# Optimization experiments

Measured on AMD Instinct MI355X. Metric: run time of the kernel, lower is better.

The kernel has to match this reference:

```python
import jax, jax.numpy as jnp
import numpy as np

EPS = 1e-5
NUM_GROUPS = 32
NUM_HEADS = 8

def group_norm(x, w, b):
    # x: (B, C, H, W), 32 groups, affine per-channel
    B, C, H, W = x.shape
    xg = x.reshape(B, NUM_GROUPS, C // NUM_GROUPS, H, W)
    mu = xg.mean(axis=(2, 3, 4), keepdims=True)
    var = xg.var(axis=(2, 3, 4), keepdims=True)
    xn = ((xg - mu) * jax.lax.rsqrt(var + EPS)).reshape(B, C, H, W)
    return xn * w[None, :, None, None] + b[None, :, None, None]

def conv1x1(x, w, b):
    # 1x1 conv == per-pixel linear; w: (out, in), x: (B, C, H, W)
    return jnp.einsum('oc,bchw->bohw', w, x) + b[None, :, None, None]

def setup_inputs() -> dict:
    key = jax.random.key(0)
    ks = jax.random.split(key, 4)
    B, C, H, W = 2, 512, 64, 64
    s = 1.0 / np.sqrt(C)
    return {
        'x': jax.random.normal(ks[0], (B, C, H, W), jnp.float32),
        'gn_w': jnp.ones((C,), jnp.float32),
        'gn_b': jnp.zeros((C,), jnp.float32),
        'wq': jax.random.normal(ks[1], (C, C), jnp.float32) * s,
        'bq': jnp.zeros((C,), jnp.float32),
        'wkv': jax.random.normal(ks[2], (2 * C, C), jnp.float32) * s,
        'bkv': jnp.zeros((2 * C,), jnp.float32),
        'wo': jax.random.normal(ks[3], (C, C), jnp.float32) * s,
        'bo': jnp.zeros((C,), jnp.float32),
    }

def reference(x, gn_w, gn_b, wq, bq, wkv, bkv, wo, bo):
    B, C, H, W = x.shape
    hd = C // NUM_HEADS  # head_dim
    residual = x
    x_norm = group_norm(x, gn_w, gn_b)
    q = conv1x1(x_norm, wq, bq).reshape(B, NUM_HEADS, hd, H * W)
    kv = conv1x1(x_norm, wkv, bkv)
    k, v = jnp.split(kv, 2, axis=1)
    k = k.reshape(B, NUM_HEADS, hd, H * W)
    v = v.reshape(B, NUM_HEADS, hd, H * W)
    scale = hd ** (-0.5)
    attn = jnp.einsum('bhdi,bhdj->bhij', q, k) * scale
    attn = jax.nn.softmax(attn, axis=-1)
    out = jnp.einsum('bhij,bhdj->bhdi', attn, v).reshape(B, C, H, W)
    out = conv1x1(out, wo, bo)
    return out + residual
```

## Files before the change

### kernel.cpp

```cpp
#include <hip/hip_runtime.h>
#include <cmath>

typedef __bf16 bf16x8 __attribute__((ext_vector_type(8)));
typedef __bf16 bf16x4 __attribute__((ext_vector_type(4)));
typedef float  f32x4  __attribute__((ext_vector_type(4)));
typedef unsigned uint2_ev __attribute__((ext_vector_type(2)));

static __device__ __forceinline__ f32x4 mfma16(bf16x8 a, bf16x8 b, f32x4 c) {
    return __builtin_amdgcn_mfma_f32_16x16x32_bf16(a, b, c, 0, 0, 0);
}

static __device__ __forceinline__ float fast_exp2(float x) {
#if __has_builtin(__builtin_amdgcn_exp2f)
    return __builtin_amdgcn_exp2f(x);
#else
    return exp2f(x);
#endif
}

static __device__ __forceinline__ void quad_swap(unsigned &a, unsigned &b) {
#if __has_builtin(__builtin_amdgcn_permlane32_swap) && __has_builtin(__builtin_amdgcn_permlane16_swap)
    uint2_ev r32 = __builtin_amdgcn_permlane32_swap(a, b, false, false);
    uint2_ev r16 = __builtin_amdgcn_permlane16_swap(r32[0], r32[1], false, false);
    a = r16[0]; b = r16[1];
#else
    asm volatile("v_permlane32_swap_b32 %0, %1\n\t"
                 "v_permlane16_swap_b32 %0, %1"
                 : "+v"(a), "+v"(b));
#endif
}

static __device__ __forceinline__ void gload_lds16(const void* g, void* l) {
    __builtin_amdgcn_global_load_lds((const __attribute__((address_space(1))) void*)g,
                                     (__attribute__((address_space(3))) void*)l, 16, 0, 0);
}

#define OFF_STATS 0
#define OFF_W     4096
#define OFF_XNT   (OFF_W + 2u*1024*1024)
#define OFF_QKT   (OFF_XNT + 8u*1024*1024)
#define OFF_V     (OFF_QKT + 16u*1024*1024)
#define OFF_OP    (OFF_V + 8u*1024*1024)
#define CHUNK_O   4194304u
#define CHUNK_L   65536u

__global__ __launch_bounds__(256) void cvt_w(const float* __restrict__ wq,
                                             const float* __restrict__ wkv,
                                             const float* __restrict__ wo,
                                             __bf16* __restrict__ dst) {
    int i = blockIdx.x * 256 + threadIdx.x;
    if (i < 262144)      dst[i] = (__bf16)wq[i];
    else if (i < 786432) dst[i] = (__bf16)wkv[i - 262144];
    else                 dst[i] = (__bf16)wo[i - 786432];
}

__global__ __launch_bounds__(256) void gn_stats(const float* __restrict__ x,
                                                float* __restrict__ stats) {
    int blk = blockIdx.x;
    int bg = blk >> 2, chunk = blk & 3;
    const float* base = x + (size_t)bg * 65536 + (size_t)chunk * 16384;
    float s = 0.f, ss = 0.f;
    for (int i = threadIdx.x; i < 4096; i += 256) {
        float4 v = ((const float4*)base)[i];
        s  += v.x + v.y + v.z + v.w;
        ss += v.x*v.x + v.y*v.y + v.z*v.z + v.w*v.w;
    }
    #pragma unroll
    for (int off = 1; off < 64; off <<= 1) {
        s  += __shfl_xor(s,  off);
        ss += __shfl_xor(ss, off);
    }
    __shared__ float red[8];
    int wave = threadIdx.x >> 6;
    if ((threadIdx.x & 63) == 0) { red[wave*2] = s; red[wave*2+1] = ss; }
    __syncthreads();
    if (threadIdx.x == 0) {
        float S  = red[0] + red[2] + red[4] + red[6];
        float SS = red[1] + red[3] + red[5] + red[7];
        atomicAdd(&stats[bg*2],     S);
        atomicAdd(&stats[bg*2 + 1], SS);
    }
}

__global__ __launch_bounds__(256) void gn_apply(const float* __restrict__ x,
                                                const float* __restrict__ stats,
                                                const float* __restrict__ w,
                                                const float* __restrict__ bgn,
                                                __bf16* __restrict__ xnT) {
    int p0 = blockIdx.x * 64, c0 = blockIdx.y * 64, b = blockIdx.z;
    int tid = threadIdx.x, lane = tid & 63, wave = tid >> 6;
    __shared__ float t[64][69];
    #pragma unroll
    for (int i = 0; i < 16; ++i) {
        int cc = i * 4 + wave;
        int c  = c0 + cc;
        int g  = (b << 5) + (c >> 4);
        float mu  = stats[g*2] * (1.f/65536.f);
        float var = stats[g*2+1] * (1.f/65536.f) - mu*mu;
        float rstd = rsqrtf(var + 1e-5f);
        float val = x[((size_t)(b*512 + c) << 12) + p0 + lane];
        t[cc][lane] = (val - mu) * rstd * w[c] + bgn[c];
    }
    __syncthreads();
    #pragma unroll
    for (int i = 0; i < 16; ++i) {
        int pp = i * 4 + wave;
        xnT[((size_t)(b*4096 + p0 + pp) << 9) + c0 + lane] = (__bf16)t[lane][pp];
    }
}

__global__ __launch_bounds__(256) void gemm128_kernel(
    const __bf16* __restrict__ A, const __bf16* __restrict__ B,
    const float* __restrict__ bias, const float* __restrict__ bias2, int nsplit,
    float scale0, void* __restrict__ out,
    int N, int K, long long strideA, long long strideO) {
    const int bz = blockIdx.z;
    A += strideA * bz;
    const int m0 = blockIdx.x * 128, n0 = blockIdx.y * 128;
    const int tid = threadIdx.x, lane = tid & 63, wave = tid >> 6;
    const int quad = lane >> 4, l16 = lane & 15;
    const int wm = (wave >> 1) * 64, wn = (wave & 1) * 64;

    __shared__ __attribute__((aligned(16))) __bf16 lds_a[128][40];
    __shared__ __attribute__((aligned(16))) __bf16 lds_b[128][40];

    f32x4 acc[4][4];
    #pragma unroll
    for (int mt = 0; mt < 4; ++mt)
        #pragma unroll
        for (int nt = 0; nt < 4; ++nt)
            #pragma unroll
            for (int r = 0; r < 4; ++r) acc[mt][nt][r] = 0.f;

    const int row_s = tid >> 2;
    const int kc    = (tid & 3) << 3;

    uint4 ra0, ra1, rb0, rb1;
    const __bf16* Abase = A + (size_t)(m0 + row_s) * K + kc;
    const __bf16* Bbase = B + (size_t)(n0 + row_s) * K + kc;
    ra0 = *(const uint4*)Abase;
    ra1 = *(const uint4*)(Abase + (size_t)64 * K);
    rb0 = *(const uint4*)Bbase;
    rb1 = *(const uint4*)(Bbase + (size_t)64 * K);

    for (int kt = 0; kt < K; kt += 32) {
        *(uint4*)&lds_a[row_s][kc]      = ra0;
        *(uint4*)&lds_a[row_s + 64][kc] = ra1;
        *(uint4*)&lds_b[row_s][kc]      = rb0;
        *(uint4*)&lds_b[row_s + 64][kc] = rb1;
        __syncthreads();
        if (kt + 32 < K) {
            ra0 = *(const uint4*)(Abase + kt + 32);
            ra1 = *(const uint4*)(Abase + kt + 32 + (size_t)64 * K);
            rb0 = *(const uint4*)(Bbase + kt + 32);
            rb1 = *(const uint4*)(Bbase + kt + 32 + (size_t)64 * K);
        }
        bf16x8 af[4], bfr[4];
        #pragma unroll
        for (int mt = 0; mt < 4; ++mt)
            af[mt] = *(const bf16x8*)&lds_a[wm + mt*16 + l16][quad*8];
        #pragma unroll
        for (int nt = 0; nt < 4; ++nt)
            bfr[nt] = *(const bf16x8*)&lds_b[wn + nt*16 + l16][quad*8];
        #pragma unroll
        for (int mt = 0; mt < 4; ++mt)
            #pragma unroll
            for (int nt = 0; nt < 4; ++nt)
                acc[mt][nt] = mfma16(af[mt], bfr[nt], acc[mt][nt]);
        __syncthreads();
    }

    #pragma unroll
    for (int mt = 0; mt < 4; ++mt) {
        const int mrow = m0 + wm + mt*16 + quad*4;
        #pragma unroll
        for (int nt = 0; nt < 4; ++nt) {
            const int ncol = n0 + wn + nt*16 + l16;
            #pragma unroll
            for (int r = 0; r < 4; ++r) {
                const int m = mrow + r;
                float bval = (ncol < nsplit) ? bias[ncol] : bias2[ncol - nsplit];
                float val = acc[mt][nt][r] + bval;
                if (ncol < nsplit) val *= scale0;
                ((__bf16*)out)[(size_t)strideO * bz + (size_t)m * N + ncol] = (__bf16)val;
            }
        }
    }
}

template<int OUT_F32, int HAS_RES>
__global__ __launch_bounds__(256) void gemm64_kernel(
    const __bf16* __restrict__ A, const __bf16* __restrict__ B,
    const float* __restrict__ bias, const float* __restrict__ res,
    void* __restrict__ out,
    int N, int K, long long strideB, long long strideO) {
    const int bz = blockIdx.z;
    B += strideB * bz;
    const int m0 = blockIdx.x * 64, n0 = blockIdx.y * 128;
    const int tid = threadIdx.x, lane = tid & 63, wave = tid >> 6;
    const int quad = lane >> 4, l16 = lane & 15;
    const int wn = wave * 32;

    __shared__ __attribute__((aligned(16))) __bf16 lds_a[64][40];
    __shared__ __attribute__((aligned(16))) __bf16 lds_b[128][40];

    f32x4 acc[4][2];
    #pragma unroll
    for (int mt = 0; mt < 4; ++mt)
        #pragma unroll
        for (int nt = 0; nt < 2; ++nt)
            #pragma unroll
            for (int r = 0; r < 4; ++r) acc[mt][nt][r] = 0.f;

    const int row_s = tid >> 2;
    const int kc    = (tid & 3) << 3;

    uint4 ra0, rb0, rb1;
    const __bf16* Abase = A + (size_t)(m0 + row_s) * K + kc;
    const __bf16* Bbase = B + (size_t)(n0 + row_s) * K + kc;
    ra0 = *(const uint4*)Abase;
    rb0 = *(const uint4*)Bbase;
    rb1 = *(const uint4*)(Bbase + (size_t)64 * K);

    for (int kt = 0; kt < K; kt += 32) {
        *(uint4*)&lds_a[row_s][kc]      = ra0;
        *(uint4*)&lds_b[row_s][kc]      = rb0;
        *(uint4*)&lds_b[row_s + 64][kc] = rb1;
        __syncthreads();
        if (kt + 32 < K) {
            ra0 = *(const uint4*)(Abase + kt + 32);
            rb0 = *(const uint4*)(Bbase + kt + 32);
            rb1 = *(const uint4*)(Bbase + kt + 32 + (size_t)64 * K);
        }
        bf16x8 af[4], bfr[2];
        #pragma unroll
        for (int mt = 0; mt < 4; ++mt)
            af[mt] = *(const bf16x8*)&lds_a[mt*16 + l16][quad*8];
        #pragma unroll
        for (int nt = 0; nt < 2; ++nt)
            bfr[nt] = *(const bf16x8*)&lds_b[wn + nt*16 + l16][quad*8];
        #pragma unroll
        for (int mt = 0; mt < 4; ++mt)
            #pragma unroll
            for (int nt = 0; nt < 2; ++nt)
                acc[mt][nt] = mfma16(af[mt], bfr[nt], acc[mt][nt]);
        __syncthreads();
    }

    #pragma unroll
    for (int mt = 0; mt < 4; ++mt) {
        const int mrow = m0 + mt*16 + quad*4;
        #pragma unroll
        for (int nt = 0; nt < 2; ++nt) {
            const int ncol = n0 + wn + nt*16 + l16;
            #pragma unroll
            for (int r = 0; r < 4; ++r) {
                const int m = mrow + r;
                float val = acc[mt][nt][r] + bias[m];
                const size_t idx = (size_t)strideO * bz + (size_t)m * N + ncol;
                if constexpr (HAS_RES) val += res[idx];
                if constexpr (OUT_F32) ((float*)out)[idx] = val;
                else ((__bf16*)out)[idx] = (__bf16)val;
            }
        }
    }
}

template<int NCH>
__global__ __launch_bounds__(256, 3) void attn_kernel(const __bf16* __restrict__ qkT,
                                                      const __bf16* __restrict__ v,
                                                      __bf16* __restrict__ attnT,
                                                      __bf16* __restrict__ Opart,
                                                      float* __restrict__ Lpart) {
    const int b = blockIdx.y >> 3, h = blockIdx.y & 7;
    const int chunk = (NCH > 1) ? blockIdx.z : 0;
    const int NITER = 64 / NCH;
    const int kt0 = chunk * (4096 / NCH);
    const int tid = threadIdx.x;
    const int wave = tid >> 6, lane = tid & 63;
    const int quad = lane >> 4, l16 = lane & 15;
    const int qbase = blockIdx.x * 256 + wave * 64;

    const __bf16* qkTb = qkT + ((size_t)b << 22);
    const __bf16* vb   = v   + ((size_t)b << 21);

    __shared__ __attribute__((aligned(16))) __bf16 lds_k[2][64][64];
    __shared__ __attribute__((aligned(16))) __bf16 lds_v[2][64][64];

    bf16x8 aq[4][2];
    #pragma unroll
    for (int mt = 0; mt < 4; ++mt) {
        const __bf16* qrow = qkTb + (size_t)(qbase + mt*16 + l16) * 1024 + h*64 + quad*8;
        aq[mt][0] = *(const bf16x8*)qrow;
        aq[mt][1] = *(const bf16x8*)(qrow + 32);
    }
    f32x4 o[4][5];
    #pragma unroll
    for (int mt = 0; mt < 4; ++mt)
        #pragma unroll
        for (int dt = 0; dt < 5; ++dt)
            #pragma unroll
            for (int r = 0; r < 4; ++r) o[mt][dt][r] = 0.f;
    const f32x4 kZero = {0.f, 0.f, 0.f, 0.f};

    bf16x8 onesb;
    #pragma unroll
    for (int e = 0; e < 8; ++e) onesb[e] = (__bf16)1.0f;

    const int myrow = (wave << 3) + (lane >> 3);
    const int mych  = ((lane & 7) ^ (myrow & 7)) << 3;
    const __bf16* kgb = qkTb + (size_t)myrow * 1024 + 512 + h*64 + mych;
    const __bf16* vgb = vb + ((size_t)(h*64 + myrow) << 12) + mych;

    auto stage = [&](int buf, int kt) {
        char* kb = (char*)(&lds_k[buf][0][0]) + (wave << 10);
        char* vp = (char*)(&lds_v[buf][0][0]) + (wave << 10);
        const __bf16* kg = kgb + (size_t)kt * 1024;
        const __bf16* vg = vgb + kt;
        gload_lds16(kg,                       kb);
        gload_lds16(kg + 32*1024,             kb + 4096);
        gload_lds16(vg,                       vp);
        gload_lds16(vg + ((size_t)32 << 12),  vp + 4096);
    };

    stage(0, kt0);

    for (int it = 0; it < NITER; ++it) {
        __syncthreads();
        const int cur = it & 1;
        if (it + 1 < NITER) stage(cur ^ 1, kt0 + (it + 1) * 64);

        #pragma unroll
        for (int kh = 0; kh < 2; ++kh) {
            unsigned pd[4][4];
            #pragma unroll
            for (int j = 0; j < 2; ++j) {
                const int nt = kh*2 + j;
                const int kr = nt*16 + l16;
                bf16x8 bk0 = *(const bf16x8*)&lds_k[cur][kr][( quad      ^ (l16 & 7)) * 8];
                bf16x8 bk1 = *(const bf16x8*)&lds_k[cur][kr][((4 + quad) ^ (l16 & 7)) * 8];
                #pragma unroll
                for (int mt = 0; mt < 4; ++mt) {
                    f32x4 s = mfma16(bk1, aq[mt][1], mfma16(bk0, aq[mt][0], kZero));
                    f32x4 p;
                    #pragma unroll
                    for (int r = 0; r < 4; ++r) p[r] = fast_exp2(s[r]);
                    bf16x4 pb = __builtin_convertvector(p, bf16x4);
                    union { bf16x4 v; unsigned d[2]; } u; u.v = pb;
                    pd[mt][j*2]     = u.d[0];
                    pd[mt][j*2 + 1] = u.d[1];
                }
            }
            bf16x8 pa[4];
            #pragma unroll
            for (int mt = 0; mt < 4; ++mt) {
                unsigned x0 = pd[mt][0], x1 = pd[mt][1];
                unsigned y0 = pd[mt][2], y1 = pd[mt][3];
                quad_swap(x0, y0);
                quad_swap(x1, y1);
                union { unsigned d[4]; bf16x8 v; } u;
                u.d[0] = x0; u.d[1] = x1; u.d[2] = y0; u.d[3] = y1;
                pa[mt] = u.v;
            }
            #pragma unroll
            for (int dt = 0; dt < 4; ++dt) {
                bf16x8 bv = *(const bf16x8*)&lds_v[cur][dt*16 + l16][((kh*4 + quad) ^ (l16 & 7)) * 8];
                #pragma unroll
                for (int mt = 0; mt < 4; ++mt)
                    o[mt][dt] = mfma16(pa[mt], bv, o[mt][dt]);
            }
            #pragma unroll
            for (int mt = 0; mt < 4; ++mt)
                o[mt][4] = mfma16(pa[mt], onesb, o[mt][4]);
        }
    }

    if constexpr (NCH > 1) {
        __bf16* Ob = Opart + (size_t)chunk * CHUNK_O;
        #pragma unroll
        for (int mt = 0; mt < 4; ++mt)
            #pragma unroll
            for (int dt = 0; dt < 4; ++dt)
                #pragma unroll
                for (int r = 0; r < 4; ++r) {
                    size_t row = (size_t)b * 4096 + qbase + mt*16 + quad*4 + r;
                    Ob[(row << 9) + (h << 6) + dt*16 + l16] = (__bf16)o[mt][dt][r];
                }
        if (l16 == 0) {
            #pragma unroll
            for (int mt = 0; mt < 4; ++mt)
                #pragma unroll
                for (int r = 0; r < 4; ++r) {
                    int p = qbase + mt*16 + quad*4 + r;
                    Lpart[(size_t)chunk * CHUNK_L + (size_t)(((b*8 + h)) << 12) + p] = o[mt][4][r];
                }
        }
    } else {
        #pragma unroll
        for (int mt = 0; mt < 4; ++mt) {
            float inv[4];
            #pragma unroll
            for (int r = 0; r < 4; ++r)
                inv[r] = 1.f / __shfl(o[mt][4][r], lane & 48);
            #pragma unroll
            for (int dt = 0; dt < 4; ++dt)
                #pragma unroll
                for (int r = 0; r < 4; ++r) {
                    size_t row = (size_t)b * 4096 + qbase + mt*16 + quad*4 + r;
                    attnT[(row << 9) + (h << 6) + dt*16 + l16] = (__bf16)(o[mt][dt][r] * inv[r]);
                }
        }
    }
}

template<int NCH>
__global__ __launch_bounds__(256) void attn_combine(const __bf16* __restrict__ Opart,
                                                    const float* __restrict__ Lpart,
                                                    __bf16* __restrict__ attnT) {
    int i = blockIdx.x * 256 + threadIdx.x;
    int c4 = i & 127;
    int p  = (i >> 7) & 4095;
    int b  = i >> 19;
    int h  = c4 >> 4;
    size_t lidx = (size_t)((b*8 + h) << 12) + p;
    float l = 0.f;
    #pragma unroll
    for (int ch = 0; ch < NCH; ++ch) l += Lpart[(size_t)ch * CHUNK_L + lidx];
    float inv = 1.f / l;
    size_t oi = ((size_t)(b*4096 + p) << 9) + c4*4;
    float acc[4] = {0.f, 0.f, 0.f, 0.f};
    #pragma unroll
    for (int ch = 0; ch < NCH; ++ch) {
        bf16x4 ov = *(const bf16x4*)&Opart[(size_t)ch * CHUNK_O + oi];
        #pragma unroll
        for (int r = 0; r < 4; ++r) acc[r] += (float)ov[r];
    }
    bf16x4 rv;
    #pragma unroll
    for (int r = 0; r < 4; ++r) rv[r] = (__bf16)(acc[r] * inv);
    *(bf16x4*)&attnT[oi] = rv;
}

extern "C" void kernel_launch(void* const* d_in, const int* in_sizes, int n_in,
                              void* d_out, int out_size, void* d_ws, size_t ws_size,
                              hipStream_t stream) {
    const float* x   = (const float*)d_in[0];
    const float* gnw = (const float*)d_in[1];
    const float* gnb = (const float*)d_in[2];
    const float* wq  = (const float*)d_in[3];
    const float* bq  = (const float*)d_in[4];
    const float* wkv = (const float*)d_in[5];
    const float* bkv = (const float*)d_in[6];
    const float* wo  = (const float*)d_in[7];
    const float* bo  = (const float*)d_in[8];
    float* out = (float*)d_out;

    char* ws = (char*)d_ws;
    float*  stats  = (float*)(ws + OFF_STATS);
    __bf16* wbf    = (__bf16*)(ws + OFF_W);
    __bf16* wkv_bf = wbf + 262144;
    __bf16* wo_bf  = wbf + 786432;
    __bf16* xnT    = (__bf16*)(ws + OFF_XNT);
    __bf16* qkT    = (__bf16*)(ws + OFF_QKT);
    __bf16* vv     = (__bf16*)(ws + OFF_V);
    __bf16* Opart  = (__bf16*)(ws + OFF_OP);
    __bf16* attnT  = xnT;

    const size_t need4 = (size_t)OFF_OP + 4u * (CHUNK_O * 2 + CHUNK_L * 4);
    const size_t need2 = (size_t)OFF_OP + 2u * (CHUNK_O * 2 + CHUNK_L * 4);
    const int nch = (ws_size >= need4) ? 4 : (ws_size >= need2 ? 2 : 1);
    float* Lpart = (float*)(ws + OFF_OP + (size_t)nch * CHUNK_O * 2);

    hipMemsetAsync(stats, 0, 512, stream);
    cvt_w<<<4096, 256, 0, stream>>>(wq, wkv, wo, wbf);
    gn_stats<<<256, 256, 0, stream>>>(x, stats);
    gn_apply<<<dim3(64, 8, 2), 256, 0, stream>>>(x, stats, gnw, gnb, xnT);

    const long long S = 2097152LL;
    const long long S2 = 4194304LL;
    gemm128_kernel<<<dim3(32, 8, 2), 256, 0, stream>>>(
        xnT, wbf, bq, bkv, 512, 0.125f * 1.44269504f, qkT, 1024, 512, S, S2);
    gemm64_kernel<0,0><<<dim3(8, 32, 2), 256, 0, stream>>>(
        wkv_bf + 262144, xnT, bkv + 512, nullptr, vv, 4096, 512, S, S);

    if (nch == 4) {
        attn_kernel<4><<<dim3(16, 16, 4), 256, 0, stream>>>(qkT, vv, nullptr, Opart, Lpart);
        attn_combine<4><<<4096, 256, 0, stream>>>(Opart, Lpart, attnT);
    } else if (nch == 2) {
        attn_kernel<2><<<dim3(16, 16, 2), 256, 0, stream>>>(qkT, vv, nullptr, Opart, Lpart);
        attn_combine<2><<<4096, 256, 0, stream>>>(Opart, Lpart, attnT);
    } else {
        attn_kernel<1><<<dim3(16, 16, 1), 256, 0, stream>>>(qkT, vv, attnT, nullptr, nullptr);
    }

    gemm64_kernel<1,1><<<dim3(8, 32, 2), 256, 0, stream>>>(
        wo_bf, attnT, bo, x, out, 4096, 512, S, S);
}
```

Baseline: 223.3 us.

## Replace ones-MFMA row sum with VALU accumulation and remap blocks per XCD

Drops the extra MFMA against a ones vector that computed the softmax denominator. It instead sums the fp32 exp values in registers and reduces them across lanes with shuffles at the end, which cuts matrix-core work by one fifth and frees accumulator registers. The block index is also remapped so that blocks sharing the same batch, head and chunk land on the same XCD, aiming for better L2 reuse of K/V. The tradeoffs are extra VALU adds in the inner loop, and a denominator summed from fp32 values rather than the bf16-rounded ones used in the numerator.

```diff
diff --git a/kernel.cpp b/kernel.cpp
--- a/kernel.cpp
+++ b/kernel.cpp
@@ -272,14 +272,19 @@
                                                       __bf16* __restrict__ attnT,
                                                       __bf16* __restrict__ Opart,
                                                       float* __restrict__ Lpart) {
-    const int b = blockIdx.y >> 3, h = blockIdx.y & 7;
-    const int chunk = (NCH > 1) ? blockIdx.z : 0;
+    const int p   = blockIdx.x + (blockIdx.y << 4) + (blockIdx.z << 8);
+    const int xcd = p & 7, seq = p >> 3;
+    const int g   = xcd * (2 * NCH) + (seq >> 4);
+    const int xq  = seq & 15;
+    const int yy  = g & 15, zz = g >> 4;
+    const int b = yy >> 3, h = yy & 7;
+    const int chunk = (NCH > 1) ? zz : 0;
     const int NITER = 64 / NCH;
     const int kt0 = chunk * (4096 / NCH);
     const int tid = threadIdx.x;
     const int wave = tid >> 6, lane = tid & 63;
     const int quad = lane >> 4, l16 = lane & 15;
-    const int qbase = blockIdx.x * 256 + wave * 64;
+    const int qbase = xq * 256 + wave * 64;
 
     const __bf16* qkTb = qkT + ((size_t)b << 22);
     const __bf16* vb   = v   + ((size_t)b << 21);
@@ -294,18 +299,15 @@
         aq[mt][0] = *(const bf16x8*)qrow;
         aq[mt][1] = *(const bf16x8*)(qrow + 32);
     }
-    f32x4 o[4][5];
+    f32x4 o[4][4];
     #pragma unroll
     for (int mt = 0; mt < 4; ++mt)
         #pragma unroll
-        for (int dt = 0; dt < 5; ++dt)
+        for (int dt = 0; dt < 4; ++dt)
             #pragma unroll
             for (int r = 0; r < 4; ++r) o[mt][dt][r] = 0.f;
+    float lsum[4] = {0.f, 0.f, 0.f, 0.f};
     const f32x4 kZero = {0.f, 0.f, 0.f, 0.f};
-
-    bf16x8 onesb;
-    #pragma unroll
-    for (int e = 0; e < 8; ++e) onesb[e] = (__bf16)1.0f;
 
     const int myrow = (wave << 3) + (lane >> 3);
     const int mych  = ((lane & 7) ^ (myrow & 7)) << 3;
@@ -342,10 +344,11 @@
                 #pragma unroll
                 for (int mt = 0; mt < 4; ++mt) {
                     f32x4 s = mfma16(bk1, aq[mt][1], mfma16(bk0, aq[mt][0], kZero));
-                    f32x4 p;
+                    f32x4 pv;
                     #pragma unroll
-                    for (int r = 0; r < 4; ++r) p[r] = fast_exp2(s[r]);
-                    bf16x4 pb = __builtin_convertvector(p, bf16x4);
+                    for (int r = 0; r < 4; ++r) pv[r] = fast_exp2(s[r]);
+                    lsum[mt] += (pv[0] + pv[1]) + (pv[2] + pv[3]);
+                    bf16x4 pb = __builtin_convertvector(pv, bf16x4);
                     union { bf16x4 v; unsigned d[2]; } u; u.v = pb;
                     pd[mt][j*2]     = u.d[0];
                     pd[mt][j*2 + 1] = u.d[1];
@@ -369,10 +372,16 @@
                 for (int mt = 0; mt < 4; ++mt)
                     o[mt][dt] = mfma16(pa[mt], bv, o[mt][dt]);
             }
-            #pragma unroll
-            for (int mt = 0; mt < 4; ++mt)
-                o[mt][4] = mfma16(pa[mt], onesb, o[mt][4]);
-        }
+        }
+    }
+
+    float fsum[4];
+    #pragma unroll
+    for (int mt = 0; mt < 4; ++mt) {
+        float fs = lsum[mt];
+        fs += __shfl_xor(fs, 16);
+        fs += __shfl_xor(fs, 32);
+        fsum[mt] = fs;
     }
 
     if constexpr (NCH > 1) {
@@ -386,14 +395,12 @@
                     size_t row = (size_t)b * 4096 + qbase + mt*16 + quad*4 + r;
                     Ob[(row << 9) + (h << 6) + dt*16 + l16] = (__bf16)o[mt][dt][r];
                 }
-        if (l16 == 0) {
-            #pragma unroll
-            for (int mt = 0; mt < 4; ++mt)
-                #pragma unroll
-                for (int r = 0; r < 4; ++r) {
-                    int p = qbase + mt*16 + quad*4 + r;
-                    Lpart[(size_t)chunk * CHUNK_L + (size_t)(((b*8 + h)) << 12) + p] = o[mt][4][r];
-                }
+        if (lane < 16) {
+            #pragma unroll
+            for (int mt = 0; mt < 4; ++mt) {
+                int pq = qbase + mt*16 + lane;
+                Lpart[(size_t)chunk * CHUNK_L + (size_t)(((b*8 + h)) << 12) + pq] = fsum[mt];
+            }
         }
     } else {
         #pragma unroll
@@ -401,7 +408,7 @@
             float inv[4];
             #pragma unroll
             for (int r = 0; r < 4; ++r)
-                inv[r] = 1.f / __shfl(o[mt][4][r], lane & 48);
+                inv[r] = 1.f / __shfl(fsum[mt], (quad << 2) + r);
             #pragma unroll
             for (int dt = 0; dt < 4; ++dt)
                 #pragma unroll
```

Result: slower. 283.5 us (+26.9%).
